# Optimization experiments

Measured on AMD Instinct MI355X. Metric: run time of the kernel, lower is better.

## Reference

```python
import jax, jax.numpy as jnp
import numpy as np

EPS = 1e-5

def _gcn_norm(edge_index, n):
    # Add self-loops, compute symmetric normalization deg^-1/2 * deg^-1/2 (PyG GCNConv).
    src = jnp.concatenate([edge_index[0], jnp.arange(n)])
    dst = jnp.concatenate([edge_index[1], jnp.arange(n)])
    deg = jax.ops.segment_sum(jnp.ones_like(dst, dtype=jnp.float32), dst, num_segments=n)
    dinv = jnp.where(deg > 0, jax.lax.rsqrt(deg), 0.0)
    norm = dinv[src] * dinv[dst]  # [E + N]
    return src, dst, norm

def _gcn_conv(x, W, b, src, dst, norm, n):
    h = x @ W                      # linear first (out_dim < in_dim here)
    msg = h[src] * norm[:, None]   # gather + per-edge scale
    out = jax.ops.segment_sum(msg, dst, num_segments=n)  # scatter-add aggregation
    return out + b

def _bn(x, g, b):
    # BatchNorm over nodes (training-mode batch statistics, biased variance)
    mu = x.mean(axis=0)
    var = jnp.mean((x - mu) ** 2, axis=0)
    return (x - mu) * jax.lax.rsqrt(var + EPS) * g + b


def setup_inputs() -> dict:
    key = jax.random.key(0)
    N, E, F_in = 10000, 320000, 256
    ks = jax.random.split(key, 8)
    dims = [F_in, 220, 150, 100, 60, 17]
    inp = {
        'x': jax.random.normal(ks[0], (N, F_in), dtype=jnp.float32),
        'edge_index': jax.random.randint(ks[1], (2, E), 0, N, dtype=jnp.int64),
    }
    for i in range(5):
        fan_in, fan_out = dims[i], dims[i + 1]
        scale = 1.0 / np.sqrt(fan_in)
        inp[f'W{i+1}'] = jax.random.normal(ks[2 + i], (fan_in, fan_out), dtype=jnp.float32) * scale
        inp[f'b{i+1}'] = jnp.zeros((fan_out,), dtype=jnp.float32)
    for i, d in enumerate([220, 150, 100, 60]):
        inp[f'g{i+1}'] = jnp.ones((d,), dtype=jnp.float32)
        inp[f'be{i+1}'] = jnp.zeros((d,), dtype=jnp.float32)
    return inp


def reference(x, edge_index, W1, b1, W2, b2, W3, b3, W4, b4, W5, b5,
              g1, be1, g2, be2, g3, be3, g4, be4):
    n = x.shape[0]
    src, dst, norm = _gcn_norm(edge_index, n)
    h = _gcn_conv(x, W1, b1, src, dst, norm, n)
    h = _bn(jax.nn.relu(h), g1, be1)
    # dropout omitted (eval-mode identity)
    h = _gcn_conv(h, W2, b2, src, dst, norm, n)
    h = _bn(jax.nn.relu(h), g2, be2)
    h = _gcn_conv(h, W3, b3, src, dst, norm, n)
    h = _bn(jax.nn.relu(h), g3, be3)
    h = _gcn_conv(h, W4, b4, src, dst, norm, n)
    h = _bn(jax.nn.relu(h), g4, be4)
    h = _gcn_conv(h, W5, b5, src, dst, norm, n)
    return jax.nn.log_softmax(h, axis=1)
```

## Files before the change

### kernel.cpp

```cpp
#include <hip/hip_runtime.h>
#include <math.h>

typedef unsigned short ushort_t;
typedef unsigned int uint_t;
typedef unsigned long long ull_t;

__device__ __forceinline__ float bf2f(ushort_t u) {
    union { uint_t i; float f; } x; x.i = ((uint_t)u) << 16; return x.f;
}
__device__ __forceinline__ ushort_t f2bf(float f) {
    union { float f; uint_t i; } x; x.f = f;
    uint_t r = x.i + 0x7FFFu + ((x.i >> 16) & 1u);
    return (ushort_t)(r >> 16);
}


__global__ void k_zero(int* __restrict__ cnt, float* __restrict__ cs,
                       float* __restrict__ csq, int n) {
    int i = blockIdx.x * blockDim.x + threadIdx.x;
    if (i < n) cnt[i] = 0;
    if (i < 256) { cs[i] = 0.f; csq[i] = 0.f; }
}

__global__ void k_hist(const int* __restrict__ dst, int* __restrict__ cnt, int E) {
    int e = blockIdx.x * blockDim.x + threadIdx.x;
    if (e < E) atomicAdd(&cnt[dst[e]], 1);
}

__global__ __launch_bounds__(1024) void k_scan(
    const int* __restrict__ cnt, int* __restrict__ row_start,
    int* __restrict__ cursor, float* __restrict__ dinv, int N)
{
    __shared__ int sh[1024];
    const int tid = threadIdx.x;
    const int chunk = (N + 1023) >> 10;
    int loc[16];
    const int base = tid * chunk;
    int sum = 0;
    for (int c = 0; c < chunk; ++c) {
        int i = base + c;
        int v = (i < N) ? cnt[i] : 0;
        loc[c] = sum;
        sum += v;
    }
    sh[tid] = sum;
    __syncthreads();
    for (int off = 1; off < 1024; off <<= 1) {
        int v = (tid >= off) ? sh[tid - off] : 0;
        __syncthreads();
        sh[tid] += v;
        __syncthreads();
    }
    const int excl = sh[tid] - sum;
    for (int c = 0; c < chunk; ++c) {
        int i = base + c;
        if (i < N) {
            int rs = excl + loc[c];
            row_start[i] = rs;
            cursor[i] = rs;
            dinv[i] = rsqrtf(1.0f + (float)cnt[i]);
        }
    }
    if (tid == 1023) row_start[N] = sh[1023];
}

__global__ void k_fill(const int* __restrict__ src, const int* __restrict__ dst,
                       int* __restrict__ cursor, int* __restrict__ csr_src, int E) {
    int e = blockIdx.x * blockDim.x + threadIdx.x;
    if (e < E) {
        int pos = atomicAdd(&cursor[dst[e]], 1);
        csr_src[pos] = src[e];
    }
}


__global__ void k_cvtx(const float* __restrict__ x, ushort_t* __restrict__ xb, int n4) {
    int i = blockIdx.x * 256 + threadIdx.x;
    if (i < n4) {
        const float4 v = ((const float4*)x)[i];
        ushort_t* o = xb + i * 4;
        o[0] = f2bf(v.x); o[1] = f2bf(v.y); o[2] = f2bf(v.z); o[3] = f2bf(v.w);
    }
}

__global__ void k_prepW(const float* __restrict__ W, const float* __restrict__ scale,
                        ushort_t* __restrict__ Wt, int K, int M, int Kp, int Mp)
{
    int k = blockIdx.x * 64 + threadIdx.x;
    int j = blockIdx.y * 4 + threadIdx.y;
    if (k >= Kp || j >= Mp) return;
    float v = 0.f;
    if (k < K && j < M) {
        float s = (scale != nullptr) ? scale[k] : 1.f;
        v = s * W[(long)k * M + j];
    }
    Wt[(long)j * Kp + k] = f2bf(v);
}

__global__ __launch_bounds__(256) void k_prepb(
    const float* __restrict__ W, const float* __restrict__ shift,
    float* __restrict__ wbias, int K, int M, int Mp)
{
    __shared__ float red[4][64];
    const int jl = threadIdx.x & 63;
    const int kg = threadIdx.x >> 6;
    const int j = blockIdx.x * 64 + jl;
    float s = 0.f;
    if (shift != nullptr && j < M) {
        for (int k = kg; k < K; k += 4) s += shift[k] * W[(long)k * M + j];
    }
    red[kg][jl] = s;
    __syncthreads();
    if (kg == 0 && j < Mp)
        wbias[j] = red[0][jl] + red[1][jl] + red[2][jl] + red[3][jl];
}

template<int KP>
__global__ __launch_bounds__(64) void k_gemm_mfma(
    const ushort_t* __restrict__ Xb, const ushort_t* __restrict__ Wt,
    const float* __restrict__ wbias, const float* __restrict__ dinv,
    ushort_t* __restrict__ h2, int N, int Mp)
{
    typedef __attribute__((ext_vector_type(8))) short short8;
    typedef __attribute__((ext_vector_type(4))) float floatx4;
    const int lane = threadIdx.x;
    const int m = lane & 15;
    const int quad = lane >> 4;
    const int i0 = blockIdx.x * 16;
    const int j0 = blockIdx.y * 64;
    const int ntiles = min(4, (Mp - j0) >> 4);

    floatx4 acc[4];
    #pragma unroll
    for (int t = 0; t < 4; ++t) { acc[t].x = 0.f; acc[t].y = 0.f; acc[t].z = 0.f; acc[t].w = 0.f; }

    const int ra = min(i0 + m, N - 1);
    const ushort_t* arow = Xb + (long)ra * KP + quad * 8;
    const ushort_t* brow = Wt + (long)(j0 + m) * KP + quad * 8;

    #pragma unroll
    for (int k0 = 0; k0 < KP; k0 += 32) {
        short8 av = *(const short8*)(arow + k0);
        #pragma unroll
        for (int t = 0; t < 4; ++t) {
            if (t < ntiles) {
                short8 bv = *(const short8*)(brow + (long)t * 16 * KP + k0);
                acc[t] = __builtin_amdgcn_mfma_f32_16x16x32_bf16(av, bv, acc[t], 0, 0, 0);
            }
        }
    }

    #pragma unroll
    for (int t = 0; t < 4; ++t) {
        if (t < ntiles) {
            int j = j0 + t * 16 + m;
            float wb = wbias[j];
            #pragma unroll
            for (int r = 0; r < 4; ++r) {
                int i = i0 + quad * 4 + r;
                if (i < N) h2[(long)i * Mp + j] = f2bf((acc[t][r] + wb) * dinv[i]);
            }
        }
    }
}

__global__ __launch_bounds__(256) void k_agg(
    const int* __restrict__ row_start, const int* __restrict__ csr_src,
    const ushort_t* __restrict__ h2, int hs,
    const float* __restrict__ dinv, const float* __restrict__ b,
    ushort_t* __restrict__ tmpb, int ts,
    int N, int M, int Q, ull_t magic, uint_t sh)
{
    const uint_t g = blockIdx.x * 256 + threadIdx.x;
    const uint_t i = (uint_t)(((ull_t)g * magic) >> sh);
    const int jp = (int)(g - i * Q);
    if (i >= (uint_t)N) return;
    const int j0 = jp * 4;
    if (j0 >= M) {
        *(uint2*)(tmpb + (long)i * ts + j0) = make_uint2(0u, 0u);
        return;
    }
    const int s0 = row_start[i];
    const int s1 = row_start[i + 1];
    const ushort_t* hp = h2 + j0;
    uint2 v = *(const uint2*)(hp + (long)i * hs);
    float a0 = bf2f((ushort_t)(v.x & 0xffff)), a1 = bf2f((ushort_t)(v.x >> 16));
    float a2 = bf2f((ushort_t)(v.y & 0xffff)), a3 = bf2f((ushort_t)(v.y >> 16));
    int e = s0;
    for (; e + 3 < s1; e += 4) {
        int n0 = csr_src[e], n1 = csr_src[e + 1], n2 = csr_src[e + 2], n3 = csr_src[e + 3];
        uint2 w0 = *(const uint2*)(hp + (long)n0 * hs);
        uint2 w1 = *(const uint2*)(hp + (long)n1 * hs);
        uint2 w2 = *(const uint2*)(hp + (long)n2 * hs);
        uint2 w3 = *(const uint2*)(hp + (long)n3 * hs);
        a0 += bf2f((ushort_t)(w0.x & 0xffff)); a1 += bf2f((ushort_t)(w0.x >> 16));
        a2 += bf2f((ushort_t)(w0.y & 0xffff)); a3 += bf2f((ushort_t)(w0.y >> 16));
        a0 += bf2f((ushort_t)(w1.x & 0xffff)); a1 += bf2f((ushort_t)(w1.x >> 16));
        a2 += bf2f((ushort_t)(w1.y & 0xffff)); a3 += bf2f((ushort_t)(w1.y >> 16));
        a0 += bf2f((ushort_t)(w2.x & 0xffff)); a1 += bf2f((ushort_t)(w2.x >> 16));
        a2 += bf2f((ushort_t)(w2.y & 0xffff)); a3 += bf2f((ushort_t)(w2.y >> 16));
        a0 += bf2f((ushort_t)(w3.x & 0xffff)); a1 += bf2f((ushort_t)(w3.x >> 16));
        a2 += bf2f((ushort_t)(w3.y & 0xffff)); a3 += bf2f((ushort_t)(w3.y >> 16));
    }
    for (; e < s1; ++e) {
        uint2 w = *(const uint2*)(hp + (long)csr_src[e] * hs);
        a0 += bf2f((ushort_t)(w.x & 0xffff)); a1 += bf2f((ushort_t)(w.x >> 16));
        a2 += bf2f((ushort_t)(w.y & 0xffff)); a3 += bf2f((ushort_t)(w.y >> 16));
    }
    const float di = dinv[i];
    float r0 = (j0     < M) ? fmaxf(a0 * di + b[j0],     0.f) : 0.f;
    float r1 = (j0 + 1 < M) ? fmaxf(a1 * di + b[j0 + 1], 0.f) : 0.f;
    float r2 = (j0 + 2 < M) ? fmaxf(a2 * di + b[j0 + 2], 0.f) : 0.f;
    float r3 = (j0 + 3 < M) ? fmaxf(a3 * di + b[j0 + 3], 0.f) : 0.f;
    uint2 pk;
    pk.x = (uint_t)f2bf(r0) | ((uint_t)f2bf(r1) << 16);
    pk.y = (uint_t)f2bf(r2) | ((uint_t)f2bf(r3) << 16);
    *(uint2*)(tmpb + (long)i * ts + j0) = pk;
}

__global__ __launch_bounds__(256) void k_agg_final(
    const int* __restrict__ row_start, const int* __restrict__ csr_src,
    const ushort_t* __restrict__ h2, const float* __restrict__ dinv,
    const float* __restrict__ b, float* __restrict__ out, int N, int M)
{
    const int x = threadIdx.x;
    const int i = blockIdx.x * 16 + threadIdx.y;
    if (i >= N) return;
    const int j0 = 2 * x, j1 = 2 * x + 1;
    uint_t v = *(const uint_t*)(h2 + (long)i * 32 + j0);
    float a0 = bf2f((ushort_t)(v & 0xffff));
    float a1 = bf2f((ushort_t)(v >> 16));
    const int s0 = row_start[i];
    const int s1 = row_start[i + 1];
    int e = s0;
    for (; e + 1 < s1; e += 2) {
        int n0 = csr_src[e], n1 = csr_src[e + 1];
        uint_t w0 = *(const uint_t*)(h2 + (long)n0 * 32 + j0);
        uint_t w1 = *(const uint_t*)(h2 + (long)n1 * 32 + j0);
        a0 += bf2f((ushort_t)(w0 & 0xffff)); a1 += bf2f((ushort_t)(w0 >> 16));
        a0 += bf2f((ushort_t)(w1 & 0xffff)); a1 += bf2f((ushort_t)(w1 >> 16));
    }
    for (; e < s1; ++e) {
        uint_t w = *(const uint_t*)(h2 + (long)csr_src[e] * 32 + j0);
        a0 += bf2f((ushort_t)(w & 0xffff)); a1 += bf2f((ushort_t)(w >> 16));
    }
    const float di = dinv[i];
    float r0 = (j0 < M) ? (a0 * di + b[j0]) : -INFINITY;
    float r1 = (j1 < M) ? (a1 * di + b[j1]) : -INFINITY;
    float m = fmaxf(r0, r1);
    #pragma unroll
    for (int msk = 1; msk < 16; msk <<= 1) m = fmaxf(m, __shfl_xor(m, msk, 16));
    float s = ((j0 < M) ? expf(r0 - m) : 0.f) + ((j1 < M) ? expf(r1 - m) : 0.f);
    #pragma unroll
    for (int msk = 1; msk < 16; msk <<= 1) s += __shfl_xor(s, msk, 16);
    const float l = logf(s) + m;
    if (j0 < M) out[(long)i * M + j0] = r0 - l;
    if (j1 < M) out[(long)i * M + j1] = r1 - l;
}

__global__ __launch_bounds__(256) void k_stats(
    const ushort_t* __restrict__ tmpb, int ts,
    float* __restrict__ cs, float* __restrict__ csq, int N)
{
    const int t = threadIdx.x;
    if (2 * t >= ts) return;
    const int i0 = blockIdx.x * 64;
    float s0 = 0.f, q0 = 0.f, s1 = 0.f, q1 = 0.f;
    for (int r = 0; r < 64; ++r) {
        int i = i0 + r;
        if (i < N) {
            uint_t w = *(const uint_t*)(tmpb + (long)i * ts + 2 * t);
            float v0 = bf2f((ushort_t)(w & 0xffff));
            float v1 = bf2f((ushort_t)(w >> 16));
            s0 += v0; q0 += v0 * v0;
            s1 += v1; q1 += v1 * v1;
        }
    }
    atomicAdd(&cs[2 * t], s0);
    atomicAdd(&csq[2 * t], q0);
    atomicAdd(&cs[2 * t + 1], s1);
    atomicAdd(&csq[2 * t + 1], q1);
}

__global__ void k_bn_finalize(
    const float* __restrict__ g, const float* __restrict__ be,
    float* __restrict__ cs, float* __restrict__ csq,
    float* __restrict__ scale, float* __restrict__ shift,
    int M, float invN)
{
    int j = threadIdx.x;
    if (j < M) {
        float mu  = cs[j] * invN;
        float var = csq[j] * invN - mu * mu;
        float sc  = g[j] * rsqrtf(var + 1e-5f);
        scale[j] = sc;
        shift[j] = be[j] - mu * sc;
    }
    if (j < 256) { cs[j] = 0.f; csq[j] = 0.f; }
}


static inline int pad16(int v) { return (v + 15) & ~15; }
static inline int pad32(int v) { return (v + 31) & ~31; }

extern "C" void kernel_launch(void* const* d_in, const int* in_sizes, int n_in,
                              void* d_out, int out_size, void* d_ws, size_t ws_size,
                              hipStream_t stream)
{
    const int dims[6] = {256, 220, 150, 100, 60, 17};
    const int N = in_sizes[0] / dims[0];
    const int E = in_sizes[1] / 2;

    const float* x  = (const float*)d_in[0];
    const int* ei   = (const int*)d_in[1];
    const int* srcv = ei;
    const int* dstv = ei + E;
    const float* Wl[5], *bl[5];
    for (int l = 0; l < 5; ++l) {
        Wl[l] = (const float*)d_in[2 + 2 * l];
        bl[l] = (const float*)d_in[3 + 2 * l];
    }
    const float* gl[4], *bel[4];
    for (int l = 0; l < 4; ++l) {
        gl[l]  = (const float*)d_in[12 + 2 * l];
        bel[l] = (const float*)d_in[13 + 2 * l];
    }
    float* out = (float*)d_out;

    char* w = (char*)d_ws;
    const long NB   = ((long)N * 4 + 255) & ~255L;
    const long NB1  = ((long)(N + 1) * 4 + 255) & ~255L;
    const long EB   = ((long)E * 4 + 255) & ~255L;
    const long XBB  = ((long)N * 256 * 2 + 255) & ~255L;
    const long FBB  = ((long)N * 224 * 2 + 255) & ~255L;
    const long WTB  = ((long)224 * 256 * 2 + 255) & ~255L;

    long o = 0;
    float* dinv      = (float*)(w + o);  o += NB;
    float* cs        = (float*)(w + o);  o += 1024;
    float* csq       = (float*)(w + o);  o += 1024;
    float* scl       = (float*)(w + o);  o += 1024;
    float* shf       = (float*)(w + o);  o += 1024;
    float* wbias     = (float*)(w + o);  o += 1024;
    int*   cnt       = (int*)(w + o);    o += NB;
    int*   row_start = (int*)(w + o);    o += NB1;
    int*   cursor    = (int*)(w + o);    o += NB;
    int*   csr_src   = (int*)(w + o);    o += EB;
    ushort_t* xb     = (ushort_t*)(w + o); o += XBB;
    ushort_t* Wt     = (ushort_t*)(w + o); o += WTB;
    ushort_t* h2     = (ushort_t*)(w + o); o += FBB;
    ushort_t* tmpb   = (ushort_t*)(w + o); o += FBB;

    const int nBlk = (N + 255) / 256;
    const int eBlk = (E + 255) / 256;

    k_zero<<<nBlk, 256, 0, stream>>>(cnt, cs, csq, N);
    k_hist<<<eBlk, 256, 0, stream>>>(dstv, cnt, E);
    k_scan<<<1, 1024, 0, stream>>>(cnt, row_start, cursor, dinv, N);
    k_fill<<<eBlk, 256, 0, stream>>>(srcv, dstv, cursor, csr_src, E);
    k_cvtx<<<(N * 64 + 255) / 256, 256, 0, stream>>>(x, xb, N * 64);

    const float invN = 1.0f / (float)N;

    for (int l = 0; l < 5; ++l) {
        const int K  = dims[l];
        const int M  = dims[l + 1];
        const int Kp = pad32(K);
        const int Mp = pad16(M);
        const int ts = (l < 4) ? pad32(M) : 32;
        const ushort_t* X = (l == 0) ? xb : tmpb;
        const float* sc_p = (l == 0) ? nullptr : scl;
        const float* sh_p = (l == 0) ? nullptr : shf;

        k_prepW<<<dim3((Kp + 63) / 64, (Mp + 3) / 4), dim3(64, 4), 0, stream>>>(
            Wl[l], sc_p, Wt, K, M, Kp, Mp);
        k_prepb<<<(Mp + 63) / 64, 256, 0, stream>>>(Wl[l], sh_p, wbias, K, M, Mp);

        dim3 gg((N + 15) / 16, (Mp + 63) / 64);
        switch (Kp) {
            case 256: k_gemm_mfma<256><<<gg, 64, 0, stream>>>(X, Wt, wbias, dinv, h2, N, Mp); break;
            case 224: k_gemm_mfma<224><<<gg, 64, 0, stream>>>(X, Wt, wbias, dinv, h2, N, Mp); break;
            case 160: k_gemm_mfma<160><<<gg, 64, 0, stream>>>(X, Wt, wbias, dinv, h2, N, Mp); break;
            case 128: k_gemm_mfma<128><<<gg, 64, 0, stream>>>(X, Wt, wbias, dinv, h2, N, Mp); break;
            case  64: k_gemm_mfma< 64><<<gg, 64, 0, stream>>>(X, Wt, wbias, dinv, h2, N, Mp); break;
        }

        if (l < 4) {
            const int Q = ts / 4;
            uint_t shmt = 0;
            while ((1u << shmt) < (uint_t)Q) ++shmt;
            shmt += 32;
            const ull_t magic = ((1ULL << shmt) + Q - 1) / (ull_t)Q;
            const long total = (long)N * Q;
            k_agg<<<(int)((total + 255) / 256), 256, 0, stream>>>(
                row_start, csr_src, h2, Mp, dinv, bl[l], tmpb, ts, N, M, Q, magic, shmt);

            k_stats<<<(N + 63) / 64, 256, 0, stream>>>(tmpb, ts, cs, csq, N);
            k_bn_finalize<<<1, 256, 0, stream>>>(gl[l], bel[l], cs, csq, scl, shf, M, invN);
        } else {
            k_agg_final<<<(N + 15) / 16, dim3(16, 16), 0, stream>>>(
                row_start, csr_src, h2, dinv, bl[l], out, N, M);
        }
    }
}
```

Before: 431.7 us.

## Fuse BN stats into aggregation and merge init/prep kernels

Folds the batch-norm column sum and sum-of-squares into the aggregation kernel. Partial sums go through shared-memory atomics and then global atomics, and a last-block counter computes the scale and shift in the same kernel. Zeroing, x conversion and layer-0 weight transposition are merged into one init kernel, and the per-layer weight and bias prep kernels are merged into one launch. This removes several launches and the re-read of the aggregated activations, at the cost of heavy shared and global atomic contention and float atomic ordering nondeterminism.

```diff
diff --git a/kernel.cpp b/kernel.cpp
--- a/kernel.cpp
+++ b/kernel.cpp
@@ -14,12 +14,30 @@
     return (ushort_t)(r >> 16);
 }
 
-
-__global__ void k_zero(int* __restrict__ cnt, float* __restrict__ cs,
-                       float* __restrict__ csq, int n) {
-    int i = blockIdx.x * blockDim.x + threadIdx.x;
-    if (i < n) cnt[i] = 0;
-    if (i < 256) { cs[i] = 0.f; csq[i] = 0.f; }
+__global__ __launch_bounds__(256) void k_init(
+    const float* __restrict__ x, const float* __restrict__ W0,
+    int* __restrict__ cnt, float* __restrict__ stats, int* __restrict__ ctr,
+    float* __restrict__ wbias, ushort_t* __restrict__ xb, ushort_t* __restrict__ Wt,
+    int N)
+{
+    const int gt = blockIdx.x * 256 + threadIdx.x;
+    const int gth = gridDim.x * 256;
+    for (int i = gt; i < N; i += gth) cnt[i] = 0;
+    for (int i = gt; i < 2048; i += gth) stats[i] = 0.f;
+    if (gt < 8) ctr[gt] = 0;
+    if (gt < 256) wbias[gt] = 0.f;
+    const int n4 = N * 64;
+    for (int i = gt; i < n4; i += gth) {
+        float4 v = ((const float4*)x)[i];
+        ushort_t* o = xb + i * 4;
+        o[0] = f2bf(v.x); o[1] = f2bf(v.y); o[2] = f2bf(v.z); o[3] = f2bf(v.w);
+    }
+    for (int idx = gt; idx < 224 * 256; idx += gth) {
+        int j = idx >> 8;
+        int k = idx & 255;
+        float v = (j < 220) ? W0[(long)k * 220 + j] : 0.f;
+        Wt[idx] = f2bf(v);
+    }
 }
 
 __global__ void k_hist(const int* __restrict__ dst, int* __restrict__ cnt, int E) {
@@ -73,46 +91,31 @@
     }
 }
 
-
-__global__ void k_cvtx(const float* __restrict__ x, ushort_t* __restrict__ xb, int n4) {
-    int i = blockIdx.x * 256 + threadIdx.x;
-    if (i < n4) {
-        const float4 v = ((const float4*)x)[i];
-        ushort_t* o = xb + i * 4;
-        o[0] = f2bf(v.x); o[1] = f2bf(v.y); o[2] = f2bf(v.z); o[3] = f2bf(v.w);
-    }
-}
-
-__global__ void k_prepW(const float* __restrict__ W, const float* __restrict__ scale,
-                        ushort_t* __restrict__ Wt, int K, int M, int Kp, int Mp)
-{
-    int k = blockIdx.x * 64 + threadIdx.x;
-    int j = blockIdx.y * 4 + threadIdx.y;
-    if (k >= Kp || j >= Mp) return;
-    float v = 0.f;
-    if (k < K && j < M) {
-        float s = (scale != nullptr) ? scale[k] : 1.f;
-        v = s * W[(long)k * M + j];
-    }
-    Wt[(long)j * Kp + k] = f2bf(v);
-}
-
-__global__ __launch_bounds__(256) void k_prepb(
-    const float* __restrict__ W, const float* __restrict__ shift,
-    float* __restrict__ wbias, int K, int M, int Mp)
-{
-    __shared__ float red[4][64];
-    const int jl = threadIdx.x & 63;
-    const int kg = threadIdx.x >> 6;
-    const int j = blockIdx.x * 64 + jl;
-    float s = 0.f;
-    if (shift != nullptr && j < M) {
-        for (int k = kg; k < K; k += 4) s += shift[k] * W[(long)k * M + j];
-    }
-    red[kg][jl] = s;
-    __syncthreads();
-    if (kg == 0 && j < Mp)
-        wbias[j] = red[0][jl] + red[1][jl] + red[2][jl] + red[3][jl];
+__global__ void k_prep(const float* __restrict__ W,
+                       const float* __restrict__ scl, const float* __restrict__ shf,
+                       ushort_t* __restrict__ Wt, float* __restrict__ wbias,
+                       int K, int M, int Kp, int Mp, int yW)
+{
+    if ((int)blockIdx.y < yW) {
+        int k = blockIdx.x * 64 + threadIdx.x;
+        int j = blockIdx.y * 4 + threadIdx.y;
+        if (k >= Kp || j >= Mp) return;
+        float v = 0.f;
+        if (k < K && j < M) v = scl[k] * W[(long)k * M + j];
+        Wt[(long)j * Kp + k] = f2bf(v);
+    } else {
+        __shared__ float red[4][64];
+        int t = threadIdx.y * 64 + threadIdx.x;
+        int jl = t & 63, kg = t >> 6;
+        int j = blockIdx.x * 64 + jl;
+        float s = 0.f;
+        if (j < M) {
+            for (int k = kg; k < K; k += 4) s += shf[k] * W[(long)k * M + j];
+        }
+        red[kg][jl] = s;
+        __syncthreads();
+        if (kg == 0 && j < Mp) wbias[j] = red[0][jl] + red[1][jl] + red[2][jl] + red[3][jl];
+    }
 }
 
 template<int KP>
@@ -164,58 +167,92 @@
     }
 }
 
-__global__ __launch_bounds__(256) void k_agg(
+__global__ __launch_bounds__(256) void k_aggstat(
     const int* __restrict__ row_start, const int* __restrict__ csr_src,
     const ushort_t* __restrict__ h2, int hs,
     const float* __restrict__ dinv, const float* __restrict__ b,
     ushort_t* __restrict__ tmpb, int ts,
-    int N, int M, int Q, ull_t magic, uint_t sh)
-{
-    const uint_t g = blockIdx.x * 256 + threadIdx.x;
-    const uint_t i = (uint_t)(((ull_t)g * magic) >> sh);
-    const int jp = (int)(g - i * Q);
-    if (i >= (uint_t)N) return;
-    const int j0 = jp * 4;
-    if (j0 >= M) {
-        *(uint2*)(tmpb + (long)i * ts + j0) = make_uint2(0u, 0u);
-        return;
-    }
-    const int s0 = row_start[i];
-    const int s1 = row_start[i + 1];
-    const ushort_t* hp = h2 + j0;
-    uint2 v = *(const uint2*)(hp + (long)i * hs);
-    float a0 = bf2f((ushort_t)(v.x & 0xffff)), a1 = bf2f((ushort_t)(v.x >> 16));
-    float a2 = bf2f((ushort_t)(v.y & 0xffff)), a3 = bf2f((ushort_t)(v.y >> 16));
-    int e = s0;
-    for (; e + 3 < s1; e += 4) {
-        int n0 = csr_src[e], n1 = csr_src[e + 1], n2 = csr_src[e + 2], n3 = csr_src[e + 3];
-        uint2 w0 = *(const uint2*)(hp + (long)n0 * hs);
-        uint2 w1 = *(const uint2*)(hp + (long)n1 * hs);
-        uint2 w2 = *(const uint2*)(hp + (long)n2 * hs);
-        uint2 w3 = *(const uint2*)(hp + (long)n3 * hs);
-        a0 += bf2f((ushort_t)(w0.x & 0xffff)); a1 += bf2f((ushort_t)(w0.x >> 16));
-        a2 += bf2f((ushort_t)(w0.y & 0xffff)); a3 += bf2f((ushort_t)(w0.y >> 16));
-        a0 += bf2f((ushort_t)(w1.x & 0xffff)); a1 += bf2f((ushort_t)(w1.x >> 16));
-        a2 += bf2f((ushort_t)(w1.y & 0xffff)); a3 += bf2f((ushort_t)(w1.y >> 16));
-        a0 += bf2f((ushort_t)(w2.x & 0xffff)); a1 += bf2f((ushort_t)(w2.x >> 16));
-        a2 += bf2f((ushort_t)(w2.y & 0xffff)); a3 += bf2f((ushort_t)(w2.y >> 16));
-        a0 += bf2f((ushort_t)(w3.x & 0xffff)); a1 += bf2f((ushort_t)(w3.x >> 16));
-        a2 += bf2f((ushort_t)(w3.y & 0xffff)); a3 += bf2f((ushort_t)(w3.y >> 16));
-    }
-    for (; e < s1; ++e) {
-        uint2 w = *(const uint2*)(hp + (long)csr_src[e] * hs);
-        a0 += bf2f((ushort_t)(w.x & 0xffff)); a1 += bf2f((ushort_t)(w.x >> 16));
-        a2 += bf2f((ushort_t)(w.y & 0xffff)); a3 += bf2f((ushort_t)(w.y >> 16));
-    }
-    const float di = dinv[i];
-    float r0 = (j0     < M) ? fmaxf(a0 * di + b[j0],     0.f) : 0.f;
-    float r1 = (j0 + 1 < M) ? fmaxf(a1 * di + b[j0 + 1], 0.f) : 0.f;
-    float r2 = (j0 + 2 < M) ? fmaxf(a2 * di + b[j0 + 2], 0.f) : 0.f;
-    float r3 = (j0 + 3 < M) ? fmaxf(a3 * di + b[j0 + 3], 0.f) : 0.f;
-    uint2 pk;
-    pk.x = (uint_t)f2bf(r0) | ((uint_t)f2bf(r1) << 16);
-    pk.y = (uint_t)f2bf(r2) | ((uint_t)f2bf(r3) << 16);
-    *(uint2*)(tmpb + (long)i * ts + j0) = pk;
+    const float* __restrict__ g, const float* __restrict__ be,
+    float* __restrict__ cs, float* __restrict__ cq, int* __restrict__ ctr,
+    float* __restrict__ scl, float* __restrict__ shf,
+    int N, int M, int Q, ull_t magic, uint_t sh, float invN)
+{
+    __shared__ float sred[448];
+    __shared__ int lastflag;
+    const int tid = threadIdx.x;
+    for (int j = tid; j < 2 * ts; j += 256) sred[j] = 0.f;
+    __syncthreads();
+
+    const uint_t gidx = blockIdx.x * 256 + tid;
+    const uint_t i = (uint_t)(((ull_t)gidx * magic) >> sh);
+    const int jp = (int)(gidx - i * Q);
+    const int j0 = jp << 2;
+    const bool active = (i < (uint_t)N);
+    if (active) {
+        if (j0 >= M) {
+            *(uint2*)(tmpb + (long)i * ts + j0) = make_uint2(0u, 0u);
+        } else {
+            const int s0 = row_start[i], s1 = row_start[i + 1];
+            const ushort_t* hp = h2 + j0;
+            uint2 v = *(const uint2*)(hp + (long)i * hs);
+            float a0 = bf2f((ushort_t)(v.x & 0xffff)), a1 = bf2f((ushort_t)(v.x >> 16));
+            float a2 = bf2f((ushort_t)(v.y & 0xffff)), a3 = bf2f((ushort_t)(v.y >> 16));
+            int e = s0;
+            for (; e + 3 < s1; e += 4) {
+                int n0 = csr_src[e], n1 = csr_src[e + 1], n2 = csr_src[e + 2], n3 = csr_src[e + 3];
+                uint2 w0 = *(const uint2*)(hp + (long)n0 * hs);
+                uint2 w1 = *(const uint2*)(hp + (long)n1 * hs);
+                uint2 w2 = *(const uint2*)(hp + (long)n2 * hs);
+                uint2 w3 = *(const uint2*)(hp + (long)n3 * hs);
+                a0 += bf2f((ushort_t)(w0.x & 0xffff)); a1 += bf2f((ushort_t)(w0.x >> 16));
+                a2 += bf2f((ushort_t)(w0.y & 0xffff)); a3 += bf2f((ushort_t)(w0.y >> 16));
+                a0 += bf2f((ushort_t)(w1.x & 0xffff)); a1 += bf2f((ushort_t)(w1.x >> 16));
+                a2 += bf2f((ushort_t)(w1.y & 0xffff)); a3 += bf2f((ushort_t)(w1.y >> 16));
+                a0 += bf2f((ushort_t)(w2.x & 0xffff)); a1 += bf2f((ushort_t)(w2.x >> 16));
+                a2 += bf2f((ushort_t)(w2.y & 0xffff)); a3 += bf2f((ushort_t)(w2.y >> 16));
+                a0 += bf2f((ushort_t)(w3.x & 0xffff)); a1 += bf2f((ushort_t)(w3.x >> 16));
+                a2 += bf2f((ushort_t)(w3.y & 0xffff)); a3 += bf2f((ushort_t)(w3.y >> 16));
+            }
+            for (; e < s1; ++e) {
+                uint2 w = *(const uint2*)(hp + (long)csr_src[e] * hs);
+                a0 += bf2f((ushort_t)(w.x & 0xffff)); a1 += bf2f((ushort_t)(w.x >> 16));
+                a2 += bf2f((ushort_t)(w.y & 0xffff)); a3 += bf2f((ushort_t)(w.y >> 16));
+            }
+            const float di = dinv[i];
+            float r0 = fmaxf(a0 * di + b[j0], 0.f);
+            float r1 = (j0 + 1 < M) ? fmaxf(a1 * di + b[j0 + 1], 0.f) : 0.f;
+            float r2 = (j0 + 2 < M) ? fmaxf(a2 * di + b[j0 + 2], 0.f) : 0.f;
+            float r3 = (j0 + 3 < M) ? fmaxf(a3 * di + b[j0 + 3], 0.f) : 0.f;
+            uint2 pk;
+            pk.x = (uint_t)f2bf(r0) | ((uint_t)f2bf(r1) << 16);
+            pk.y = (uint_t)f2bf(r2) | ((uint_t)f2bf(r3) << 16);
+            *(uint2*)(tmpb + (long)i * ts + j0) = pk;
+            atomicAdd(&sred[j0], r0);          atomicAdd(&sred[ts + j0], r0 * r0);
+            atomicAdd(&sred[j0 + 1], r1);      atomicAdd(&sred[ts + j0 + 1], r1 * r1);
+            atomicAdd(&sred[j0 + 2], r2);      atomicAdd(&sred[ts + j0 + 2], r2 * r2);
+            atomicAdd(&sred[j0 + 3], r3);      atomicAdd(&sred[ts + j0 + 3], r3 * r3);
+        }
+    }
+    __syncthreads();
+    for (int j = tid; j < M; j += 256) {
+        atomicAdd(&cs[j], sred[j]);
+        atomicAdd(&cq[j], sred[ts + j]);
+    }
+    __threadfence();
+    __syncthreads();
+    if (tid == 0) lastflag = (atomicAdd(ctr, 1) == (int)gridDim.x - 1) ? 1 : 0;
+    __syncthreads();
+    if (lastflag) {
+        if (tid < M) {
+            float csv = atomicAdd(&cs[tid], 0.f);
+            float cqv = atomicAdd(&cq[tid], 0.f);
+            float mu = csv * invN;
+            float var = cqv * invN - mu * mu;
+            float sc = g[tid] * rsqrtf(var + 1e-5f);
+            scl[tid] = sc;
+            shf[tid] = be[tid] - mu * sc;
+        }
+    }
 }
 
 __global__ __launch_bounds__(256) void k_agg_final(
@@ -258,47 +295,6 @@
     if (j1 < M) out[(long)i * M + j1] = r1 - l;
 }
 
-__global__ __launch_bounds__(256) void k_stats(
-    const ushort_t* __restrict__ tmpb, int ts,
-    float* __restrict__ cs, float* __restrict__ csq, int N)
-{
-    const int t = threadIdx.x;
-    if (2 * t >= ts) return;
-    const int i0 = blockIdx.x * 64;
-    float s0 = 0.f, q0 = 0.f, s1 = 0.f, q1 = 0.f;
-    for (int r = 0; r < 64; ++r) {
-        int i = i0 + r;
-        if (i < N) {
-            uint_t w = *(const uint_t*)(tmpb + (long)i * ts + 2 * t);
-            float v0 = bf2f((ushort_t)(w & 0xffff));
-            float v1 = bf2f((ushort_t)(w >> 16));
-            s0 += v0; q0 += v0 * v0;
-            s1 += v1; q1 += v1 * v1;
-        }
-    }
-    atomicAdd(&cs[2 * t], s0);
-    atomicAdd(&csq[2 * t], q0);
-    atomicAdd(&cs[2 * t + 1], s1);
-    atomicAdd(&csq[2 * t + 1], q1);
-}
-
-__global__ void k_bn_finalize(
-    const float* __restrict__ g, const float* __restrict__ be,
-    float* __restrict__ cs, float* __restrict__ csq,
-    float* __restrict__ scale, float* __restrict__ shift,
-    int M, float invN)
-{
-    int j = threadIdx.x;
-    if (j < M) {
-        float mu  = cs[j] * invN;
-        float var = csq[j] * invN - mu * mu;
-        float sc  = g[j] * rsqrtf(var + 1e-5f);
-        scale[j] = sc;
-        shift[j] = be[j] - mu * sc;
-    }
-    if (j < 256) { cs[j] = 0.f; csq[j] = 0.f; }
-}
-
 
 static inline int pad16(int v) { return (v + 15) & ~15; }
 static inline int pad32(int v) { return (v + 31) & ~31; }
@@ -328,20 +324,20 @@
     float* out = (float*)d_out;
 
     char* w = (char*)d_ws;
-    const long NB   = ((long)N * 4 + 255) & ~255L;
-    const long NB1  = ((long)(N + 1) * 4 + 255) & ~255L;
-    const long EB   = ((long)E * 4 + 255) & ~255L;
-    const long XBB  = ((long)N * 256 * 2 + 255) & ~255L;
-    const long FBB  = ((long)N * 224 * 2 + 255) & ~255L;
-    const long WTB  = ((long)224 * 256 * 2 + 255) & ~255L;
+    const long NB  = ((long)N * 4 + 255) & ~255L;
+    const long NB1 = ((long)(N + 1) * 4 + 255) & ~255L;
+    const long EB  = ((long)E * 4 + 255) & ~255L;
+    const long XBB = ((long)N * 256 * 2 + 255) & ~255L;
+    const long FBB = ((long)N * 224 * 2 + 255) & ~255L;
+    const long WTB = ((long)224 * 256 * 2 + 255) & ~255L;
 
     long o = 0;
     float* dinv      = (float*)(w + o);  o += NB;
-    float* cs        = (float*)(w + o);  o += 1024;
-    float* csq       = (float*)(w + o);  o += 1024;
+    float* stats     = (float*)(w + o);  o += 2048 * 4;
     float* scl       = (float*)(w + o);  o += 1024;
     float* shf       = (float*)(w + o);  o += 1024;
     float* wbias     = (float*)(w + o);  o += 1024;
+    int*   ctr       = (int*)(w + o);    o += 256;
     int*   cnt       = (int*)(w + o);    o += NB;
     int*   row_start = (int*)(w + o);    o += NB1;
     int*   cursor    = (int*)(w + o);    o += NB;
@@ -351,16 +347,14 @@
     ushort_t* h2     = (ushort_t*)(w + o); o += FBB;
     ushort_t* tmpb   = (ushort_t*)(w + o); o += FBB;
 
-    const int nBlk = (N + 255) / 256;
     const int eBlk = (E + 255) / 256;
-
-    k_zero<<<nBlk, 256, 0, stream>>>(cnt, cs, csq, N);
+    const float invN = 1.0f / (float)N;
+
+    k_init<<<(N * 64 + 255) / 256, 256, 0, stream>>>(x, Wl[0], cnt, stats, ctr,
+                                                     wbias, xb, Wt, N);
     k_hist<<<eBlk, 256, 0, stream>>>(dstv, cnt, E);
     k_scan<<<1, 1024, 0, stream>>>(cnt, row_start, cursor, dinv, N);
     k_fill<<<eBlk, 256, 0, stream>>>(srcv, dstv, cursor, csr_src, E);
-    k_cvtx<<<(N * 64 + 255) / 256, 256, 0, stream>>>(x, xb, N * 64);
-
-    const float invN = 1.0f / (float)N;
 
     for (int l = 0; l < 5; ++l) {
         const int K  = dims[l];
@@ -369,12 +363,12 @@
         const int Mp = pad16(M);
         const int ts = (l < 4) ? pad32(M) : 32;
         const ushort_t* X = (l == 0) ? xb : tmpb;
-        const float* sc_p = (l == 0) ? nullptr : scl;
-        const float* sh_p = (l == 0) ? nullptr : shf;
-
-        k_prepW<<<dim3((Kp + 63) / 64, (Mp + 3) / 4), dim3(64, 4), 0, stream>>>(
-            Wl[l], sc_p, Wt, K, M, Kp, Mp);
-        k_prepb<<<(Mp + 63) / 64, 256, 0, stream>>>(Wl[l], sh_p, wbias, K, M, Mp);
+
+        if (l > 0) {
+            const int yW = (Mp + 3) / 4;
+            k_prep<<<dim3((Kp + 63) / 64, yW + 1), dim3(64, 4), 0, stream>>>(
+                Wl[l], scl, shf, Wt, wbias, K, M, Kp, Mp, yW);
+        }
 
         dim3 gg((N + 15) / 16, (Mp + 63) / 64);
         switch (Kp) {
@@ -392,11 +386,10 @@
             shmt += 32;
             const ull_t magic = ((1ULL << shmt) + Q - 1) / (ull_t)Q;
             const long total = (long)N * Q;
-            k_agg<<<(int)((total + 255) / 256), 256, 0, stream>>>(
-                row_start, csr_src, h2, Mp, dinv, bl[l], tmpb, ts, N, M, Q, magic, shmt);
-
-            k_stats<<<(N + 63) / 64, 256, 0, stream>>>(tmpb, ts, cs, csq, N);
-            k_bn_finalize<<<1, 256, 0, stream>>>(gl[l], bel[l], cs, csq, scl, shf, M, invN);
+            k_aggstat<<<(int)((total + 255) / 256), 256, 0, stream>>>(
+                row_start, csr_src, h2, Mp, dinv, bl[l], tmpb, ts,
+                gl[l], bel[l], stats + l * 512, stats + l * 512 + 256, ctr + l,
+                scl, shf, N, M, Q, magic, shmt, invN);
         } else {
             k_agg_final<<<(N + 15) / 16, dim3(16, 16), 0, stream>>>(
                 row_start, csr_src, h2, dinv, bl[l], out, N, M);
```

Result: slower. 652.9 us (+51.2%).
